# Optimization experiments

Measured on AMD Instinct MI355X. Metric: run time of the kernel, lower is better.

Reference implementation:

```python
import jax, jax.numpy as jnp
import numpy as np

NUM_USERS = 1024
NUM_BUSINESSES = 2048
N_NODES = NUM_USERS + NUM_BUSINESSES  # 3072
B = 1024            # batch size (== NUM_USERS to keep the business_idx-offset bug valid)
E = 16384           # edges (self loops added inside reference, PyG GATConv default)
H = 768             # hidden_size
HEADS = 8
NUM_IMAGES = 3


def setup_inputs() -> dict:
    key = jax.random.key(0)
    ks = jax.random.split(key, 24)
    def rn(k, shape, s=0.02):
        return jax.random.normal(k, shape, dtype=jnp.float32) * s
    inp = {
        'text_cls': rn(ks[0], (B, 768), 1.0),              # BERT CLS features
        'img_cls': rn(ks[1], (B, NUM_IMAGES, 768), 1.0),   # ViT CLS features per image
        'biz_feats': rn(ks[2], (B, 3), 1.0),
        'W_text': rn(ks[3], (768, H)), 'b_text': jnp.zeros((H,), jnp.float32),
        'W_img': rn(ks[4], (768, H)), 'b_img': jnp.zeros((H,), jnp.float32),
        'W_bf': rn(ks[5], (3, H)), 'b_bf': jnp.zeros((H,), jnp.float32),
        'user_table': rn(ks[6], (NUM_USERS, H)),
        'biz_table': rn(ks[7], (NUM_BUSINESSES, H)),
        'W1': rn(ks[8], (H, HEADS * H)),
        'att_src1': rn(ks[9], (HEADS, H), 0.1),
        'att_dst1': rn(ks[10], (HEADS, H), 0.1),
        'b1': jnp.zeros((HEADS * H,), jnp.float32),
        'W2': rn(ks[11], (HEADS * H, H)),
        'att_src2': rn(ks[12], (1, H), 0.1),
        'att_dst2': rn(ks[13], (1, H), 0.1),
        'b2': jnp.zeros((H,), jnp.float32),
        'Wf1': rn(ks[14], (4 * H, 2 * H)), 'bf1': jnp.zeros((2 * H,), jnp.float32),
        'Wf2': rn(ks[15], (2 * H, H)), 'bf2': jnp.zeros((H,), jnp.float32),
        'Wf3': rn(ks[16], (H, 1)), 'bf3': jnp.zeros((1,), jnp.float32),
        'user_idx': jax.random.randint(ks[17], (B,), 0, NUM_USERS),
        'business_idx': jax.random.randint(ks[18], (B,), NUM_USERS, N_NODES),
        'edge_index': jax.random.randint(ks[19], (2, E), 0, N_NODES),
    }
    return inp


def gat_conv(x, src, dst, W, a_src, a_dst, bias, heads):
    # PyG GATConv: linear -> per-head additive attention -> scatter softmax over dst -> scatter add
    N = x.shape[0]
    C = W.shape[1] // heads
    h = (x @ W).reshape(N, heads, C)                       # [N,H,C]
    s_src = jnp.sum(h * a_src, axis=-1)                    # [N,H]
    s_dst = jnp.sum(h * a_dst, axis=-1)                    # [N,H]
    e = jax.nn.leaky_relu(s_src[src] + s_dst[dst], 0.2)    # [E,H]
    e_max = jax.ops.segment_max(e, dst, num_segments=N)    # [N,H]
    ee = jnp.exp(e - e_max[dst])
    denom = jax.ops.segment_sum(ee, dst, num_segments=N)   # [N,H]
    alpha = ee / (denom[dst] + 1e-16)                      # [E,H]
    out = jax.ops.segment_sum(h[src] * alpha[..., None], dst, num_segments=N)  # [N,H,C]
    return out.reshape(N, heads * C) + bias


def reference(text_cls, img_cls, biz_feats, W_text, b_text, W_img, b_img, W_bf, b_bf,
              user_table, biz_table, W1, att_src1, att_dst1, b1, W2, att_src2, att_dst2, b2,
              Wf1, bf1, Wf2, bf2, Wf3, bf3, user_idx, business_idx, edge_index):
    text_emb = text_cls @ W_text + b_text                       # TextEncoder.fc
    img_emb = jnp.mean(img_cls, axis=1) @ W_img + b_img         # ImageEncoder mean + fc
    meta = biz_feats @ W_bf + b_bf                              # business_feature_fc
    user_emb = user_table[user_idx]
    biz_emb = biz_table[business_idx - user_idx.shape[0]]       # faithful: offset by batch size
    x = jnp.zeros((N_NODES, H), jnp.float32)
    x = x.at[user_idx].set(user_emb)
    x = x.at[business_idx].set((text_emb + img_emb + meta + biz_emb) / 4.0)
    loop = jnp.arange(N_NODES)
    src = jnp.concatenate([edge_index[0], loop])                # add self loops (PyG default)
    dst = jnp.concatenate([edge_index[1], loop])
    x = jax.nn.relu(gat_conv(x, src, dst, W1, att_src1, att_dst1, b1, HEADS))
    x = gat_conv(x, src, dst, W2, att_src2, att_dst2, b2, 1)
    cat = jnp.concatenate([x[user_idx], x[business_idx], text_emb, img_emb], axis=1)  # [B,4H]
    h1 = jax.nn.relu(cat @ Wf1 + bf1)
    h2 = jax.nn.relu(h1 @ Wf2 + bf2)
    return (h2 @ Wf3 + bf3).squeeze(-1)                         # [B]
```

## Files before the change

### kernel.cpp

```cpp
#include <hip/hip_runtime.h>
#include <hip/hip_bf16.h>

namespace {

constexpr int kB = 1024;
constexpr int kNU = 1024;
constexpr int kNB = 2048;
constexpr int kNN = 3072;
constexpr int kE = 16384;
constexpr int kET = kE + kNN;
constexpr int kH = 768;
constexpr int kHeads = 8;
constexpr int kSplitK = 4;

typedef __attribute__((ext_vector_type(8))) short bf16x8_t;
typedef __attribute__((ext_vector_type(4))) float f32x4_t;

__device__ __forceinline__ float tof(float x) { return x; }
__device__ __forceinline__ float tof(__hip_bfloat16 x) { return __bfloat162float(x); }
__device__ __forceinline__ void stor(float* p, float v) { *p = v; }
__device__ __forceinline__ void stor(__hip_bfloat16* p, float v) { *p = __float2bfloat16(v); }

__device__ __forceinline__ float blo(unsigned u) {
  union { unsigned u; float f; } c; c.u = u << 16; return c.f;
}
__device__ __forceinline__ float bhi(unsigned u) {
  union { unsigned u; float f; } c; c.u = u & 0xffff0000u; return c.f;
}

__device__ __forceinline__ unsigned pk2(float a, float b) {
  union { __hip_bfloat16 h[2]; unsigned u; } c;
  c.h[0] = __float2bfloat16(a); c.h[1] = __float2bfloat16(b);
  return c.u;
}

__device__ __forceinline__ void gload_lds16(const void* g, void* l) {
  __builtin_amdgcn_global_load_lds(
      (const __attribute__((address_space(1))) void*)g,
      (__attribute__((address_space(3))) void*)l, 16, 0, 0);
}

template <int BM, int BN, int FM, int FN, typename TC>
__device__ __forceinline__ void gemm_body(
    const __hip_bfloat16* __restrict__ A, const __hip_bfloat16* __restrict__ Bt,
    const float* __restrict__ bias, TC* __restrict__ C,
    int K, int lda, int ldc, int act, int bx, int by) {
  __shared__ __align__(16) __hip_bfloat16 As[2][BM][32];
  __shared__ __align__(16) __hip_bfloat16 Bs[2][BN][32];
  const int t = threadIdx.x;
  const int w = t >> 6, lane = t & 63;
  const int wm = w >> 1, wn = w & 1;
  const int bm = by * BM, bn = bx * BN;
  const int lr = lane & 15, lg = lane >> 4;

  f32x4_t acc[FM][FN];
#pragma unroll
  for (int m = 0; m < FM; ++m)
#pragma unroll
    for (int n = 0; n < FN; ++n) acc[m][n] = (f32x4_t){0.f, 0.f, 0.f, 0.f};

  auto stage = [&](int buf, int kt) {
    const int k0 = kt << 5;
#pragma unroll
    for (int i = 0; i < BM / 64; ++i) {
      int L = i * 256 + t;
      gload_lds16(A + (size_t)(bm + (L >> 2)) * lda + k0 + (L & 3) * 8,
                  (char*)(&As[buf][0][0]) + ((size_t)(i * 256 + w * 64)) * 16);
    }
#pragma unroll
    for (int i = 0; i < BN / 64; ++i) {
      int L = i * 256 + t;
      gload_lds16(Bt + (size_t)(bn + (L >> 2)) * K + k0 + (L & 3) * 8,
                  (char*)(&Bs[buf][0][0]) + ((size_t)(i * 256 + w * 64)) * 16);
    }
  };

  const int NT = K >> 5;
  stage(0, 0);
  __syncthreads();
  for (int kt = 0; kt < NT; ++kt) {
    const int cur = kt & 1;
    if (kt + 1 < NT) stage(cur ^ 1, kt + 1);
    bf16x8_t af[FM], bv[FN];
#pragma unroll
    for (int m = 0; m < FM; ++m)
      af[m] = *(const bf16x8_t*)&As[cur][wm * FM * 16 + m * 16 + lr][lg * 8];
#pragma unroll
    for (int n = 0; n < FN; ++n)
      bv[n] = *(const bf16x8_t*)&Bs[cur][wn * FN * 16 + n * 16 + lr][lg * 8];
#pragma unroll
    for (int m = 0; m < FM; ++m)
#pragma unroll
      for (int n = 0; n < FN; ++n)
        acc[m][n] = __builtin_amdgcn_mfma_f32_16x16x32_bf16(af[m], bv[n], acc[m][n], 0, 0, 0);
    __syncthreads();
  }

#pragma unroll
  for (int m = 0; m < FM; ++m) {
    const int row0 = bm + wm * FM * 16 + m * 16 + lg * 4;
#pragma unroll
    for (int n = 0; n < FN; ++n) {
      const int cn = bn + wn * FN * 16 + n * 16 + lr;
      const float bvv = bias ? bias[cn] : 0.f;
#pragma unroll
      for (int r = 0; r < 4; ++r) {
        float v = acc[m][n][r] + bvv;
        if (act) v = fmaxf(v, 0.f);
        stor(&C[(size_t)(row0 + r) * ldc + cn], v);
      }
    }
  }
}

__device__ __forceinline__ void swz_xy(bool mfast, int& bx, int& by) {
  const int nwg = gridDim.x * gridDim.y;
  const int orig = blockIdx.y * gridDim.x + blockIdx.x;
  const int swz = (orig & 7) * (nwg >> 3) + (orig >> 3);
  if (mfast) { by = swz % gridDim.y; bx = swz / gridDim.y; }
  else       { bx = swz % gridDim.x; by = swz / gridDim.x; }
}

template <int BM, int BN, int FM, int FN, typename TC, bool MFAST>
__global__ __launch_bounds__(256) void mfma_gemm(
    const __hip_bfloat16* __restrict__ A, const __hip_bfloat16* __restrict__ Bt,
    const float* __restrict__ bias, TC* __restrict__ C,
    int N, int K, int act) {
  int bx, by;
  swz_xy(MFAST, bx, by);
  gemm_body<BM, BN, FM, FN, TC>(A, Bt, bias, C, K, K, N, act, bx, by);
}

template <int BM, int BN, int FM, int FN>
__global__ __launch_bounds__(256) void mfma_gemm_dual(
    const __hip_bfloat16* __restrict__ A0, const __hip_bfloat16* __restrict__ Bt0,
    const float* __restrict__ bias0, float* __restrict__ C0,
    const __hip_bfloat16* __restrict__ A1, const __hip_bfloat16* __restrict__ Bt1,
    const float* __restrict__ bias1, float* __restrict__ C1,
    int N, int K) {
  int bx, by;
  swz_xy(true, bx, by);
  const __hip_bfloat16* A = blockIdx.z ? A1 : A0;
  const __hip_bfloat16* Bt = blockIdx.z ? Bt1 : Bt0;
  const float* bias = blockIdx.z ? bias1 : bias0;
  float* C = blockIdx.z ? C1 : C0;
  gemm_body<BM, BN, FM, FN, float>(A, Bt, bias, C, K, K, N, 0, bx, by);
}

template <int BM, int BN, int FM, int FN>
__global__ __launch_bounds__(256) void gemm_head(
    const __hip_bfloat16* __restrict__ y, const __hip_bfloat16* __restrict__ W1t,
    const float* __restrict__ b1, __hip_bfloat16* __restrict__ x2) {
  int bx, by;
  swz_xy(true, bx, by);
  const int hd = blockIdx.z;
  gemm_body<BM, BN, FM, FN, __hip_bfloat16>(
      y + (size_t)hd * kH, W1t + (size_t)hd * kH * kH, b1 + hd * kH,
      x2 + (size_t)hd * kH, kH, kHeads * kH, kHeads * kH, 1, bx, by);
}

template <int BM, int BN, int FM, int FN>
__global__ __launch_bounds__(256) void mfma_gemm_splitk(
    const __hip_bfloat16* __restrict__ A, const __hip_bfloat16* __restrict__ Bt,
    float* __restrict__ Cpart, int M, int N, int K, int KC) {
  __shared__ __align__(16) __hip_bfloat16 As[2][BM][32];
  __shared__ __align__(16) __hip_bfloat16 Bs[2][BN][32];
  int bx, by;
  swz_xy(false, bx, by);
  const int t = threadIdx.x;
  const int w = t >> 6, lane = t & 63;
  const int wm = w >> 1, wn = w & 1;
  const int bm = by * BM, bn = bx * BN;
  const int kbeg = blockIdx.z * KC;
  const int lr = lane & 15, lg = lane >> 4;

  f32x4_t acc[FM][FN];
#pragma unroll
  for (int m = 0; m < FM; ++m)
#pragma unroll
    for (int n = 0; n < FN; ++n) acc[m][n] = (f32x4_t){0.f, 0.f, 0.f, 0.f};

  auto stage = [&](int buf, int kt) {
    const int k0 = kbeg + (kt << 5);
#pragma unroll
    for (int i = 0; i < BM / 64; ++i) {
      int L = i * 256 + t;
      gload_lds16(A + (size_t)(bm + (L >> 2)) * K + k0 + (L & 3) * 8,
                  (char*)(&As[buf][0][0]) + ((size_t)(i * 256 + w * 64)) * 16);
    }
#pragma unroll
    for (int i = 0; i < BN / 64; ++i) {
      int L = i * 256 + t;
      gload_lds16(Bt + (size_t)(bn + (L >> 2)) * K + k0 + (L & 3) * 8,
                  (char*)(&Bs[buf][0][0]) + ((size_t)(i * 256 + w * 64)) * 16);
    }
  };

  const int NT = KC >> 5;
  stage(0, 0);
  __syncthreads();
  for (int kt = 0; kt < NT; ++kt) {
    const int cur = kt & 1;
    if (kt + 1 < NT) stage(cur ^ 1, kt + 1);
    bf16x8_t af[FM], bv[FN];
#pragma unroll
    for (int m = 0; m < FM; ++m)
      af[m] = *(const bf16x8_t*)&As[cur][wm * FM * 16 + m * 16 + lr][lg * 8];
#pragma unroll
    for (int n = 0; n < FN; ++n)
      bv[n] = *(const bf16x8_t*)&Bs[cur][wn * FN * 16 + n * 16 + lr][lg * 8];
#pragma unroll
    for (int m = 0; m < FM; ++m)
#pragma unroll
      for (int n = 0; n < FN; ++n)
        acc[m][n] = __builtin_amdgcn_mfma_f32_16x16x32_bf16(af[m], bv[n], acc[m][n], 0, 0, 0);
    __syncthreads();
  }

  float* Cp = Cpart + (size_t)blockIdx.z * M * N;
#pragma unroll
  for (int m = 0; m < FM; ++m) {
    const int row0 = bm + wm * FM * 16 + m * 16 + lg * 4;
#pragma unroll
    for (int n = 0; n < FN; ++n) {
      const int cn = bn + wn * FN * 16 + n * 16 + lr;
#pragma unroll
      for (int r = 0; r < 4; ++r) Cp[(size_t)(row0 + r) * N + cn] = acc[m][n][r];
    }
  }
}

__global__ __launch_bounds__(192) void reduce_scores2_kernel(
    const float* __restrict__ part, const float* __restrict__ att_src,
    const float* __restrict__ att_dst, __hip_bfloat16* __restrict__ h2,
    float* __restrict__ s_src, float* __restrict__ s_dst) {
  __shared__ float redS[3], redD[3];
  const int row = blockIdx.x;
  const int t = threadIdx.x;
  const int c = t * 4;
  const float* p = part + (size_t)row * kH + c;
  float4 s = *(const float4*)p;
#pragma unroll
  for (int z = 1; z < kSplitK; ++z) {
    float4 qv = *(const float4*)(p + (size_t)z * kNN * kH);
    s.x += qv.x; s.y += qv.y; s.z += qv.z; s.w += qv.w;
  }
  __hip_bfloat16 b0 = __float2bfloat16(s.x), b1 = __float2bfloat16(s.y);
  __hip_bfloat16 b2 = __float2bfloat16(s.z), b3 = __float2bfloat16(s.w);
  __hip_bfloat16* o = h2 + (size_t)row * kH + c;
  o[0] = b0; o[1] = b1; o[2] = b2; o[3] = b3;
  float f0 = tof(b0), f1 = tof(b1), f2 = tof(b2), f3 = tof(b3);
  float ss = f0 * att_src[c] + f1 * att_src[c + 1] + f2 * att_src[c + 2] + f3 * att_src[c + 3];
  float sd = f0 * att_dst[c] + f1 * att_dst[c + 1] + f2 * att_dst[c + 2] + f3 * att_dst[c + 3];
#pragma unroll
  for (int off = 32; off; off >>= 1) { ss += __shfl_down(ss, off); sd += __shfl_down(sd, off); }
  if ((t & 63) == 0) { redS[t >> 6] = ss; redD[t >> 6] = sd; }
  __syncthreads();
  if (t == 0) {
    s_src[row] = redS[0] + redS[1] + redS[2];
    s_dst[row] = redD[0] + redD[1] + redD[2];
  }
}

struct TJobs {
  const float* in[6];
  __hip_bfloat16* out[6];
  int K[6];
  int N[6];
  int start[7];
};

__global__ __launch_bounds__(256) void transp_prep_kernel(
    TJobs j, const float* __restrict__ text_cls, const float* __restrict__ img_cls,
    __hip_bfloat16* __restrict__ text_bf, __hip_bfloat16* __restrict__ imgm_bf) {
  __shared__ float tl[32][33];
  const int bid = blockIdx.x;
  const int t = threadIdx.x;
  if (bid >= j.start[6]) {
    int idx = (bid - j.start[6]) * 256 + t;
    if (idx < kB * kH) {
      text_bf[idx] = __float2bfloat16(text_cls[idx]);
      int b = idx / kH, c = idx - b * kH;
      const float* p = img_cls + (size_t)b * 3 * kH + c;
      imgm_bf[idx] = __float2bfloat16((p[0] + p[kH] + p[2 * kH]) * (1.f / 3.f));
    }
    return;
  }
  int idx = 0;
#pragma unroll
  for (int q = 1; q < 6; ++q)
    if (bid >= j.start[q]) idx = q;
  const int tile = bid - j.start[idx];
  const int N = j.N[idx], K = j.K[idx];
  const int tilesN = N >> 5;
  const int n0 = (tile % tilesN) << 5, k0 = (tile / tilesN) << 5;
  const float* in = j.in[idx];
  __hip_bfloat16* out = j.out[idx];
  const int r = t >> 3, c = (t & 7) * 4;
#pragma unroll
  for (int i = 0; i < 4; ++i) tl[r][c + i] = in[(size_t)(k0 + r) * N + n0 + c + i];
  __syncthreads();
  __hip_bfloat16* op = out + (size_t)(n0 + r) * K + k0 + c;
#pragma unroll
  for (int i = 0; i < 4; ++i) op[i] = __float2bfloat16(tl[c + i][r]);
}

__global__ __launch_bounds__(256) void wa1_kernel(const float* __restrict__ W1,
                                                  const float* __restrict__ a_src,
                                                  const float* __restrict__ a_dst,
                                                  float* __restrict__ wa) {
  int gw = (blockIdx.x * 256 + threadIdx.x) >> 6;
  int lane = threadIdx.x & 63;
  if (gw >= kHeads * kH) return;
  int i = gw >> 3, hd = gw & 7;
  const float* wrow = W1 + (size_t)i * (kHeads * kH) + hd * kH;
  const float* as = a_src + (size_t)hd * kH;
  const float* ad = a_dst + (size_t)hd * kH;
  float ss = 0.f, sd = 0.f;
  for (int c = lane; c < kH; c += 64) {
    float wv = wrow[c];
    ss = fmaf(wv, as[c], ss);
    sd = fmaf(wv, ad[c], sd);
  }
#pragma unroll
  for (int o = 32; o; o >>= 1) { ss += __shfl_down(ss, o); sd += __shfl_down(sd, o); }
  if (lane == 0) {
    wa[hd * kH + i] = ss;
    wa[kHeads * kH + hd * kH + i] = sd;
  }
}

__global__ __launch_bounds__(256) void s1_kernel(const __hip_bfloat16* __restrict__ xb,
                                                 const float* __restrict__ wa,
                                                 float* __restrict__ s1s,
                                                 float* __restrict__ s1d) {
  __shared__ unsigned xrow[kH / 2];
  const int n = blockIdx.x;
  const int t = threadIdx.x;
  const unsigned* xp = (const unsigned*)(xb + (size_t)n * kH);
  if (t < 128) { xrow[t] = xp[t]; xrow[t + 128] = xp[t + 128]; xrow[t + 256] = xp[t + 256]; }
  __syncthreads();
  const int w = t >> 6, lane = t & 63;
  const float* ws0 = wa + (size_t)w * kH;
  const float* wd0 = wa + (size_t)(kHeads + w) * kH;
  const float* ws1 = wa + (size_t)(w + 4) * kH;
  const float* wd1 = wa + (size_t)(kHeads + w + 4) * kH;
  float s0 = 0.f, d0 = 0.f, s1 = 0.f, d1 = 0.f;
  for (int u = lane; u < kH / 2; u += 64) {
    unsigned v = xrow[u];
    float f0 = blo(v), f1 = bhi(v);
    int c = u * 2;
    s0 = fmaf(f0, ws0[c], fmaf(f1, ws0[c + 1], s0));
    d0 = fmaf(f0, wd0[c], fmaf(f1, wd0[c + 1], d0));
    s1 = fmaf(f0, ws1[c], fmaf(f1, ws1[c + 1], s1));
    d1 = fmaf(f0, wd1[c], fmaf(f1, wd1[c + 1], d1));
  }
#pragma unroll
  for (int o = 32; o; o >>= 1) {
    s0 += __shfl_down(s0, o); d0 += __shfl_down(d0, o);
    s1 += __shfl_down(s1, o); d1 += __shfl_down(d1, o);
  }
  if (lane == 0) {
    s1s[n * 8 + w] = s0;     s1d[n * 8 + w] = d0;
    s1s[n * 8 + w + 4] = s1; s1d[n * 8 + w + 4] = d1;
  }
}

__global__ __launch_bounds__(256) void agg1x_kernel(
    const int* __restrict__ rowptr, const int* __restrict__ cols,
    const float* __restrict__ s1s, const float* __restrict__ s1d,
    const __hip_bfloat16* __restrict__ xb, __hip_bfloat16* __restrict__ y) {
  __shared__ float mh[8], rdh[8], sdl[8];
  __shared__ float alph[128][9];
  const int n = blockIdx.x;
  const int t = threadIdx.x, w = t >> 6, lane = t & 63;
  const int beg = rowptr[n], end = rowptr[n + 1];
  if (t < 8) sdl[t] = s1d[n * 8 + t];
  __syncthreads();
#pragma unroll
  for (int p = 0; p < 2; ++p) {
    const int h = w + p * 4;
    const float sd = sdl[h];
    float m = -3.402823466e38f;
    for (int i = beg + lane; i < end; i += 64) {
      float e = s1s[(size_t)cols[i] * 8 + h] + sd;
      e = (e > 0.f) ? e : 0.2f * e;
      m = fmaxf(m, e);
    }
#pragma unroll
    for (int o = 32; o; o >>= 1) m = fmaxf(m, __shfl_xor(m, o));
    float ds = 0.f;
    for (int i = beg + lane; i < end; i += 64) {
      float e = s1s[(size_t)cols[i] * 8 + h] + sd;
      e = (e > 0.f) ? e : 0.2f * e;
      ds += expf(e - m);
    }
#pragma unroll
    for (int o = 32; o; o >>= 1) ds += __shfl_xor(ds, o);
    if (lane == 0) { mh[h] = m; rdh[h] = 1.f / (ds + 1e-16f); }
  }
  __syncthreads();

  float acc[8][4];
#pragma unroll
  for (int h = 0; h < 8; ++h)
#pragma unroll
    for (int q = 0; q < 4; ++q) acc[h][q] = 0.f;
  const int c0 = t * 4;

  for (int chunk = beg; chunk < end; chunk += 128) {
    const int cnt = min(128, end - chunk);
#pragma unroll
    for (int p = 0; p < 2; ++p) {
      const int h = w + p * 4;
      const float sd = sdl[h], m = mh[h], rd = rdh[h];
      for (int i = lane; i < cnt; i += 64) {
        float e = s1s[(size_t)cols[chunk + i] * 8 + h] + sd;
        e = (e > 0.f) ? e : 0.2f * e;
        alph[i][h] = expf(e - m) * rd;
      }
    }
    __syncthreads();
    if (t < 192) {
      for (int i = 0; i < cnt; ++i) {
        int src = cols[chunk + i];
        uint2 v = *(const uint2*)(xb + (size_t)src * kH + c0);
        float f0 = blo(v.x), f1 = bhi(v.x), f2 = blo(v.y), f3 = bhi(v.y);
#pragma unroll
        for (int h = 0; h < 8; ++h) {
          float a = alph[i][h];
          acc[h][0] = fmaf(a, f0, acc[h][0]);
          acc[h][1] = fmaf(a, f1, acc[h][1]);
          acc[h][2] = fmaf(a, f2, acc[h][2]);
          acc[h][3] = fmaf(a, f3, acc[h][3]);
        }
      }
    }
    __syncthreads();
  }
  if (t < 192) {
#pragma unroll
    for (int h = 0; h < 8; ++h) {
      uint2 o;
      o.x = pk2(acc[h][0], acc[h][1]);
      o.y = pk2(acc[h][2], acc[h][3]);
      *(uint2*)(y + ((size_t)n * 8 + h) * kH + c0) = o;
    }
  }
}

__global__ void init_kernel(uint4* __restrict__ xb4, int* __restrict__ deg,
                            int* __restrict__ winner) {
  int i = blockIdx.x * 256 + threadIdx.x;
  if (i < kNN * kH * 2 / 16) xb4[i] = (uint4){0u, 0u, 0u, 0u};
  if (i < kNN) deg[i] = 0;
  if (i < kNB) winner[i] = -1;
}

__global__ void deg_winner_kernel(const int* __restrict__ ei, int* __restrict__ deg,
                                  const int* __restrict__ business_idx,
                                  int* __restrict__ winner) {
  int e = blockIdx.x * 256 + threadIdx.x;
  if (e < kET) {
    int dst = (e < kE) ? ei[kE + e] : (e - kE);
    atomicAdd(&deg[dst], 1);
  }
  if (e < kB) atomicMax(&winner[business_idx[e] - kNU], e);
}

__global__ __launch_bounds__(1024) void scan_kernel(const int* __restrict__ deg,
                                                    int* __restrict__ rowptr,
                                                    int* __restrict__ cursor) {
  __shared__ int sums[1024];
  int t = threadIdx.x;
  int v0 = deg[t * 3], v1 = deg[t * 3 + 1], v2 = deg[t * 3 + 2];
  int s = v0 + v1 + v2;
  sums[t] = s;
  __syncthreads();
  for (int o = 1; o < 1024; o <<= 1) {
    int xv = (t >= o) ? sums[t - o] : 0;
    __syncthreads();
    sums[t] += xv;
    __syncthreads();
  }
  int excl = sums[t] - s;
  rowptr[t * 3] = excl;          cursor[t * 3] = excl;
  rowptr[t * 3 + 1] = excl + v0; cursor[t * 3 + 1] = excl + v0;
  rowptr[t * 3 + 2] = excl + v0 + v1; cursor[t * 3 + 2] = excl + v0 + v1;
  if (t == 1023) rowptr[kNN] = excl + s;
}

__global__ void fill_kernel(const int* __restrict__ ei, int* __restrict__ cursor,
                            int* __restrict__ cols) {
  int e = blockIdx.x * 256 + threadIdx.x;
  if (e >= kET) return;
  int src, dst;
  if (e < kE) { src = ei[e]; dst = ei[kE + e]; } else { src = dst = e - kE; }
  int pos = atomicAdd(&cursor[dst], 1);
  cols[pos] = src;
}

__global__ void build_x_kernel(const int* __restrict__ user_idx,
                               const float* __restrict__ user_table,
                               const int* __restrict__ winner,
                               const float* __restrict__ text_emb,
                               const float* __restrict__ img_emb,
                               const float* __restrict__ biz_feats,
                               const float* __restrict__ W_bf,
                               const float* __restrict__ b_bf,
                               const float* __restrict__ biz_table,
                               __hip_bfloat16* __restrict__ xb) {
  int b = blockIdx.x;
  if (b < kNU) {
    int node = user_idx[b];
    for (int c = threadIdx.x; c < kH; c += blockDim.x)
      xb[(size_t)node * kH + c] = __float2bfloat16(user_table[(size_t)node * kH + c]);
  } else {
    int m = b - kNU;
    int w = winner[m];
    if (w < 0) return;
    int node = kNU + m;
    float f0 = biz_feats[w * 3], f1 = biz_feats[w * 3 + 1], f2 = biz_feats[w * 3 + 2];
    for (int c = threadIdx.x; c < kH; c += blockDim.x) {
      float meta = f0 * W_bf[c] + f1 * W_bf[kH + c] + f2 * W_bf[2 * kH + c] + b_bf[c];
      float v = (text_emb[(size_t)w * kH + c] + img_emb[(size_t)w * kH + c] + meta +
                 biz_table[(size_t)m * kH + c]) * 0.25f;
      xb[(size_t)node * kH + c] = __float2bfloat16(v);
    }
  }
}

__global__ __launch_bounds__(256) void gat_agg_kernel(
    const int* __restrict__ rowptr, const int* __restrict__ cols,
    const float* __restrict__ s_src, const float* __restrict__ s_dst,
    const __hip_bfloat16* __restrict__ h, const float* __restrict__ bias,
    float* __restrict__ out_f, int total) {
  const int pair = blockIdx.x * 4 + (threadIdx.x >> 6);
  if (pair >= total) return;
  const int lane = threadIdx.x & 63;
  const int n = pair;
  const int beg = rowptr[n], end = rowptr[n + 1];
  const float sdv = s_dst[pair];

  float m = -3.402823466e38f;
  for (int i = beg + lane; i < end; i += 64) {
    float e = s_src[cols[i]] + sdv;
    e = (e > 0.f) ? e : 0.2f * e;
    m = fmaxf(m, e);
  }
#pragma unroll
  for (int o = 32; o; o >>= 1) m = fmaxf(m, __shfl_xor(m, o));

  float dsum = 0.f;
  for (int i = beg + lane; i < end; i += 64) {
    float e = s_src[cols[i]] + sdv;
    e = (e > 0.f) ? e : 0.2f * e;
    dsum += expf(e - m);
  }
#pragma unroll
  for (int o = 32; o; o >>= 1) dsum += __shfl_xor(dsum, o);
  const float rdsum = 1.f / (dsum + 1e-16f);

  float a[12];
#pragma unroll
  for (int q = 0; q < 12; ++q) a[q] = 0.f;
  const size_t hoff = (size_t)lane * 4;
  for (int i = beg; i < end; ++i) {
    int src = cols[i];
    float e = s_src[src] + sdv;
    e = (e > 0.f) ? e : 0.2f * e;
    float wgt = expf(e - m) * rdsum;
    const __hip_bfloat16* hp = h + (size_t)src * kH + hoff;
#pragma unroll
    for (int j = 0; j < 3; ++j) {
      uint2 v = *(const uint2*)(hp + j * 256);
      a[j * 4 + 0] = fmaf(wgt, blo(v.x), a[j * 4 + 0]);
      a[j * 4 + 1] = fmaf(wgt, bhi(v.x), a[j * 4 + 1]);
      a[j * 4 + 2] = fmaf(wgt, blo(v.y), a[j * 4 + 2]);
      a[j * 4 + 3] = fmaf(wgt, bhi(v.y), a[j * 4 + 3]);
    }
  }
  const size_t ob = (size_t)n * kH + hoff;
#pragma unroll
  for (int j = 0; j < 3; ++j) {
#pragma unroll
    for (int q = 0; q < 4; ++q)
      out_f[ob + j * 256 + q] = a[j * 4 + q] + bias[hoff + j * 256 + q];
  }
}

__global__ void cat_kernel(const float* __restrict__ xf, const float* __restrict__ text_emb,
                           const float* __restrict__ img_emb, const int* __restrict__ user_idx,
                           const int* __restrict__ business_idx, __hip_bfloat16* __restrict__ cat) {
  int b = blockIdx.x;
  int u = user_idx[b], z = business_idx[b];
  __hip_bfloat16* crow = cat + (size_t)b * 4 * kH;
  for (int c = threadIdx.x; c < kH; c += blockDim.x) {
    crow[c] = __float2bfloat16(xf[(size_t)u * kH + c]);
    crow[kH + c] = __float2bfloat16(xf[(size_t)z * kH + c]);
    crow[2 * kH + c] = __float2bfloat16(text_emb[(size_t)b * kH + c]);
    crow[3 * kH + c] = __float2bfloat16(img_emb[(size_t)b * kH + c]);
  }
}

__global__ __launch_bounds__(256) void final_kernel(const float* __restrict__ m2,
                                                    const float* __restrict__ Wf3,
                                                    const float* __restrict__ bf3,
                                                    float* __restrict__ out) {
  int b = (blockIdx.x * 256 + threadIdx.x) >> 6;
  int lane = threadIdx.x & 63;
  if (b >= kB) return;
  float s = 0.f;
  for (int c = lane; c < kH; c += 64) s = fmaf(m2[(size_t)b * kH + c], Wf3[c], s);
#pragma unroll
  for (int o = 32; o; o >>= 1) s += __shfl_down(s, o);
  if (lane == 0) out[b] = s + bf3[0];
}

}

extern "C" void kernel_launch(void* const* d_in, const int* in_sizes, int n_in,
                              void* d_out, int out_size, void* d_ws, size_t ws_size,
                              hipStream_t stream) {
  const float* text_cls = (const float*)d_in[0];
  const float* img_cls = (const float*)d_in[1];
  const float* biz_feats = (const float*)d_in[2];
  const float* W_text = (const float*)d_in[3];
  const float* b_text = (const float*)d_in[4];
  const float* W_img = (const float*)d_in[5];
  const float* b_img = (const float*)d_in[6];
  const float* W_bf = (const float*)d_in[7];
  const float* b_bf = (const float*)d_in[8];
  const float* user_table = (const float*)d_in[9];
  const float* biz_table = (const float*)d_in[10];
  const float* W1 = (const float*)d_in[11];
  const float* att_src1 = (const float*)d_in[12];
  const float* att_dst1 = (const float*)d_in[13];
  const float* b1 = (const float*)d_in[14];
  const float* W2 = (const float*)d_in[15];
  const float* att_src2 = (const float*)d_in[16];
  const float* att_dst2 = (const float*)d_in[17];
  const float* b2 = (const float*)d_in[18];
  const float* Wf1 = (const float*)d_in[19];
  const float* bf1 = (const float*)d_in[20];
  const float* Wf2 = (const float*)d_in[21];
  const float* bf2 = (const float*)d_in[22];
  const float* Wf3 = (const float*)d_in[23];
  const float* bf3 = (const float*)d_in[24];
  const int* user_idx = (const int*)d_in[25];
  const int* business_idx = (const int*)d_in[26];
  const int* edge_index = (const int*)d_in[27];
  float* out = (float*)d_out;
  (void)in_sizes; (void)n_in; (void)out_size; (void)ws_size;

  char* base = (char*)d_ws;
  size_t off = 0;
  auto alloc = [&](size_t bytes) -> void* {
    void* p = base + off;
    off = (off + bytes + 255) & ~(size_t)255;
    return p;
  };
  __hip_bfloat16* xb = (__hip_bfloat16*)alloc((size_t)kNN * kH * 2);
  __hip_bfloat16* text_bf = (__hip_bfloat16*)alloc((size_t)kB * kH * 2);
  __hip_bfloat16* imgm_bf = (__hip_bfloat16*)alloc((size_t)kB * kH * 2);
  float* text_emb = (float*)alloc((size_t)kB * kH * 4);
  float* img_emb = (float*)alloc((size_t)kB * kH * 4);
  __hip_bfloat16* Wtt = (__hip_bfloat16*)alloc((size_t)kH * kH * 2);
  __hip_bfloat16* Wit = (__hip_bfloat16*)alloc((size_t)kH * kH * 2);
  __hip_bfloat16* W1t = (__hip_bfloat16*)alloc((size_t)kHeads * kH * kH * 2);
  __hip_bfloat16* W2t = (__hip_bfloat16*)alloc((size_t)kH * kHeads * kH * 2);
  __hip_bfloat16* Wf1t = (__hip_bfloat16*)alloc((size_t)2 * kH * 4 * kH * 2);
  __hip_bfloat16* Wf2t = (__hip_bfloat16*)alloc((size_t)kH * 2 * kH * 2);
  float* wa = (float*)alloc((size_t)2 * kHeads * kH * 4);
  __hip_bfloat16* y = (__hip_bfloat16*)alloc((size_t)kNN * kHeads * kH * 2);
  __hip_bfloat16* x2 = (__hip_bfloat16*)alloc((size_t)kNN * kHeads * kH * 2);
  __hip_bfloat16* h2 = (__hip_bfloat16*)alloc((size_t)kNN * kH * 2);
  float* xf = (float*)alloc((size_t)kNN * kH * 4);
  float* s1s = (float*)alloc((size_t)kNN * kHeads * 4);
  float* s1d = (float*)alloc((size_t)kNN * kHeads * 4);
  float* s2s = (float*)alloc((size_t)kNN * 4);
  float* s2d = (float*)alloc((size_t)kNN * 4);
  __hip_bfloat16* catb = (__hip_bfloat16*)alloc((size_t)kB * 4 * kH * 2);
  __hip_bfloat16* m1 = (__hip_bfloat16*)alloc((size_t)kB * 2 * kH * 2);
  float* m2 = (float*)alloc((size_t)kB * kH * 4);
  int* deg = (int*)alloc((size_t)kNN * 4);
  int* rowptr = (int*)alloc((size_t)(kNN + 1) * 4);
  int* cursor = (int*)alloc((size_t)kNN * 4);
  int* cols = (int*)alloc((size_t)kET * 4);
  int* winner = (int*)alloc((size_t)kNB * 4);

  float* part = (float*)y;

  init_kernel<<<(kNN * kH * 2 / 16 + 255) / 256, 256, 0, stream>>>((uint4*)xb, deg, winner);

  TJobs tj;
  tj.in[0] = W_text; tj.out[0] = Wtt;  tj.K[0] = kH;          tj.N[0] = kH;
  tj.in[1] = W_img;  tj.out[1] = Wit;  tj.K[1] = kH;          tj.N[1] = kH;
  tj.in[2] = W1;     tj.out[2] = W1t;  tj.K[2] = kH;          tj.N[2] = kHeads * kH;
  tj.in[3] = W2;     tj.out[3] = W2t;  tj.K[3] = kHeads * kH; tj.N[3] = kH;
  tj.in[4] = Wf1;    tj.out[4] = Wf1t; tj.K[4] = 4 * kH;      tj.N[4] = 2 * kH;
  tj.in[5] = Wf2;    tj.out[5] = Wf2t; tj.K[5] = 2 * kH;      tj.N[5] = kH;
  tj.start[0] = 0;
  for (int q = 0; q < 6; ++q)
    tj.start[q + 1] = tj.start[q] + (tj.K[q] / 32) * (tj.N[q] / 32);
  const int prep_blocks = (kB * kH + 255) / 256;
  transp_prep_kernel<<<tj.start[6] + prep_blocks, 256, 0, stream>>>(tj, text_cls, img_cls,
                                                                    text_bf, imgm_bf);

  wa1_kernel<<<(kHeads * kH) / 4, 256, 0, stream>>>(W1, att_src1, att_dst1, wa);

  mfma_gemm_dual<64, 128, 2, 4><<<dim3(kH / 128, kB / 64, 2), 256, 0, stream>>>(
      text_bf, Wtt, b_text, text_emb, imgm_bf, Wit, b_img, img_emb, kH, kH);

  deg_winner_kernel<<<(kET + 255) / 256, 256, 0, stream>>>(edge_index, deg, business_idx, winner);
  scan_kernel<<<1, 1024, 0, stream>>>(deg, rowptr, cursor);
  fill_kernel<<<(kET + 255) / 256, 256, 0, stream>>>(edge_index, cursor, cols);

  build_x_kernel<<<kNN, 256, 0, stream>>>(user_idx, user_table, winner, text_emb, img_emb,
                                          biz_feats, W_bf, b_bf, biz_table, xb);

  s1_kernel<<<kNN, 256, 0, stream>>>(xb, wa, s1s, s1d);
  agg1x_kernel<<<kNN, 256, 0, stream>>>(rowptr, cols, s1s, s1d, xb, y);
  gemm_head<128, 128, 4, 4><<<dim3(kH / 128, kNN / 128, kHeads), 256, 0, stream>>>(
      y, W1t, b1, x2);

  mfma_gemm_splitk<64, 128, 2, 4><<<dim3(kH / 128, kNN / 64, kSplitK), 256, 0, stream>>>(
      x2, W2t, part, kNN, kH, kHeads * kH, kHeads * kH / kSplitK);
  reduce_scores2_kernel<<<kNN, 192, 0, stream>>>(part, att_src2, att_dst2, h2, s2s, s2d);
  gat_agg_kernel<<<kNN / 4, 256, 0, stream>>>(rowptr, cols, s2s, s2d, h2, b2, xf, kNN);

  cat_kernel<<<kB, 256, 0, stream>>>(xf, text_emb, img_emb, user_idx, business_idx, catb);
  mfma_gemm<64, 128, 2, 4, __hip_bfloat16, true><<<dim3(2 * kH / 128, kB / 64), 256, 0, stream>>>(
      catb, Wf1t, bf1, m1, 2 * kH, 4 * kH, 1);
  mfma_gemm<64, 64, 2, 2, float, true><<<dim3(kH / 64, kB / 64), 256, 0, stream>>>(
      m1, Wf2t, bf2, m2, kH, 2 * kH, 1);
  final_kernel<<<(kB * 64 + 255) / 256, 256, 0, stream>>>(m2, Wf3, bf3, out);
}
```

Measured before the change: 305.7 us.

## Split-K the MLP head GEMMs, fuse final dot, merge wa1 into prep kernel

Replaces the two MLP-head GEMMs with split-K (2-way) GEMMs writing fp32 partials, adds a reduce+bias+relu kernel after the first and a reduce+bias+relu+Wf3-dot kernel that replaces the separate final kernel. The wa1 attention-weight precompute is folded into the transpose/prep launch as extra blocks, and gemm_head's grid is reordered so heads are the fastest-varying block index. The aim is more blocks for the small 1024-row GEMMs, fewer launches, and different L2 locality for the head GEMM. The cost is extra fp32 partial traffic and reduction passes.

```diff
diff --git a/kernel.cpp b/kernel.cpp
--- a/kernel.cpp
+++ b/kernel.cpp
@@ -151,9 +151,10 @@
 __global__ __launch_bounds__(256) void gemm_head(
     const __hip_bfloat16* __restrict__ y, const __hip_bfloat16* __restrict__ W1t,
     const float* __restrict__ b1, __hip_bfloat16* __restrict__ x2) {
-  int bx, by;
-  swz_xy(true, bx, by);
-  const int hd = blockIdx.z;
+  const int hd = blockIdx.x;
+  const int tile = blockIdx.y;
+  const int bx = tile % (kH / BN);
+  const int by = tile / (kH / BN);
   gemm_body<BM, BN, FM, FN, __hip_bfloat16>(
       y + (size_t)hd * kH, W1t + (size_t)hd * kH * kH, b1 + hd * kH,
       x2 + (size_t)hd * kH, kH, kHeads * kH, kHeads * kH, 1, bx, by);
@@ -262,6 +263,47 @@
   }
 }
 
+__global__ void reduce_relu_kernel(const float* __restrict__ part,
+                                   const float* __restrict__ bias,
+                                   __hip_bfloat16* __restrict__ outb, int MN4, int N) {
+  int i = blockIdx.x * 256 + threadIdx.x;
+  if (i >= MN4) return;
+  float4 s = ((const float4*)part)[i];
+  float4 p = ((const float4*)part)[(size_t)MN4 + i];
+  int c = (i * 4) % N;
+  float v0 = fmaxf(s.x + p.x + bias[c], 0.f);
+  float v1 = fmaxf(s.y + p.y + bias[c + 1], 0.f);
+  float v2 = fmaxf(s.z + p.z + bias[c + 2], 0.f);
+  float v3 = fmaxf(s.w + p.w + bias[c + 3], 0.f);
+  uint2 o;
+  o.x = pk2(v0, v1); o.y = pk2(v2, v3);
+  *(uint2*)(outb + (size_t)i * 4) = o;
+}
+
+__global__ __launch_bounds__(192) void reduce_final_kernel(
+    const float* __restrict__ part, const float* __restrict__ bias,
+    const float* __restrict__ Wf3, const float* __restrict__ bf3,
+    float* __restrict__ out) {
+  __shared__ float red[3];
+  const int row = blockIdx.x;
+  const int t = threadIdx.x;
+  const int c = t * 4;
+  const float* p0 = part + (size_t)row * kH + c;
+  const float* p1 = p0 + (size_t)kB * kH;
+  float4 a = *(const float4*)p0;
+  float4 b = *(const float4*)p1;
+  float v0 = fmaxf(a.x + b.x + bias[c], 0.f);
+  float v1 = fmaxf(a.y + b.y + bias[c + 1], 0.f);
+  float v2 = fmaxf(a.z + b.z + bias[c + 2], 0.f);
+  float v3 = fmaxf(a.w + b.w + bias[c + 3], 0.f);
+  float s = v0 * Wf3[c] + v1 * Wf3[c + 1] + v2 * Wf3[c + 2] + v3 * Wf3[c + 3];
+#pragma unroll
+  for (int off = 32; off; off >>= 1) s += __shfl_down(s, off);
+  if ((t & 63) == 0) red[t >> 6] = s;
+  __syncthreads();
+  if (t == 0) out[row] = red[0] + red[1] + red[2] + bf3[0];
+}
+
 struct TJobs {
   const float* in[6];
   __hip_bfloat16* out[6];
@@ -272,10 +314,34 @@
 
 __global__ __launch_bounds__(256) void transp_prep_kernel(
     TJobs j, const float* __restrict__ text_cls, const float* __restrict__ img_cls,
-    __hip_bfloat16* __restrict__ text_bf, __hip_bfloat16* __restrict__ imgm_bf) {
+    __hip_bfloat16* __restrict__ text_bf, __hip_bfloat16* __restrict__ imgm_bf,
+    int prep_blocks, const float* __restrict__ W1, const float* __restrict__ a_src,
+    const float* __restrict__ a_dst, float* __restrict__ wa) {
   __shared__ float tl[32][33];
   const int bid = blockIdx.x;
   const int t = threadIdx.x;
+  if (bid >= j.start[6] + prep_blocks) {
+    int gw = ((bid - j.start[6] - prep_blocks) * 256 + t) >> 6;
+    int lane = t & 63;
+    if (gw >= kHeads * kH) return;
+    int i = gw >> 3, hd = gw & 7;
+    const float* wrow = W1 + (size_t)i * (kHeads * kH) + hd * kH;
+    const float* as = a_src + (size_t)hd * kH;
+    const float* ad = a_dst + (size_t)hd * kH;
+    float ss = 0.f, sd = 0.f;
+    for (int c = lane; c < kH; c += 64) {
+      float wv = wrow[c];
+      ss = fmaf(wv, as[c], ss);
+      sd = fmaf(wv, ad[c], sd);
+    }
+#pragma unroll
+    for (int o = 32; o; o >>= 1) { ss += __shfl_down(ss, o); sd += __shfl_down(sd, o); }
+    if (lane == 0) {
+      wa[hd * kH + i] = ss;
+      wa[kHeads * kH + hd * kH + i] = sd;
+    }
+    return;
+  }
   if (bid >= j.start[6]) {
     int idx = (bid - j.start[6]) * 256 + t;
     if (idx < kB * kH) {
@@ -303,31 +369,6 @@
   __hip_bfloat16* op = out + (size_t)(n0 + r) * K + k0 + c;
 #pragma unroll
   for (int i = 0; i < 4; ++i) op[i] = __float2bfloat16(tl[c + i][r]);
-}
-
-__global__ __launch_bounds__(256) void wa1_kernel(const float* __restrict__ W1,
-                                                  const float* __restrict__ a_src,
-                                                  const float* __restrict__ a_dst,
-                                                  float* __restrict__ wa) {
-  int gw = (blockIdx.x * 256 + threadIdx.x) >> 6;
-  int lane = threadIdx.x & 63;
-  if (gw >= kHeads * kH) return;
-  int i = gw >> 3, hd = gw & 7;
-  const float* wrow = W1 + (size_t)i * (kHeads * kH) + hd * kH;
-  const float* as = a_src + (size_t)hd * kH;
-  const float* ad = a_dst + (size_t)hd * kH;
-  float ss = 0.f, sd = 0.f;
-  for (int c = lane; c < kH; c += 64) {
-    float wv = wrow[c];
-    ss = fmaf(wv, as[c], ss);
-    sd = fmaf(wv, ad[c], sd);
-  }
-#pragma unroll
-  for (int o = 32; o; o >>= 1) { ss += __shfl_down(ss, o); sd += __shfl_down(sd, o); }
-  if (lane == 0) {
-    wa[hd * kH + i] = ss;
-    wa[kHeads * kH + hd * kH + i] = sd;
-  }
 }
 
 __global__ __launch_bounds__(256) void s1_kernel(const __hip_bfloat16* __restrict__ xb,
@@ -601,20 +642,6 @@
     crow[2 * kH + c] = __float2bfloat16(text_emb[(size_t)b * kH + c]);
     crow[3 * kH + c] = __float2bfloat16(img_emb[(size_t)b * kH + c]);
   }
-}
-
-__global__ __launch_bounds__(256) void final_kernel(const float* __restrict__ m2,
-                                                    const float* __restrict__ Wf3,
-                                                    const float* __restrict__ bf3,
-                                                    float* __restrict__ out) {
-  int b = (blockIdx.x * 256 + threadIdx.x) >> 6;
-  int lane = threadIdx.x & 63;
-  if (b >= kB) return;
-  float s = 0.f;
-  for (int c = lane; c < kH; c += 64) s = fmaf(m2[(size_t)b * kH + c], Wf3[c], s);
-#pragma unroll
-  for (int o = 32; o; o >>= 1) s += __shfl_down(s, o);
-  if (lane == 0) out[b] = s + bf3[0];
 }
 
 }
@@ -688,6 +715,7 @@
   int* cursor = (int*)alloc((size_t)kNN * 4);
   int* cols = (int*)alloc((size_t)kET * 4);
   int* winner = (int*)alloc((size_t)kNB * 4);
+  (void)m2;
 
   float* part = (float*)y;
 
@@ -704,10 +732,9 @@
   for (int q = 0; q < 6; ++q)
     tj.start[q + 1] = tj.start[q] + (tj.K[q] / 32) * (tj.N[q] / 32);
   const int prep_blocks = (kB * kH + 255) / 256;
-  transp_prep_kernel<<<tj.start[6] + prep_blocks, 256, 0, stream>>>(tj, text_cls, img_cls,
-                                                                    text_bf, imgm_bf);
-
-  wa1_kernel<<<(kHeads * kH) / 4, 256, 0, stream>>>(W1, att_src1, att_dst1, wa);
+  const int wa_blocks = (kHeads * kH) / 4;
+  transp_prep_kernel<<<tj.start[6] + prep_blocks + wa_blocks, 256, 0, stream>>>(
+      tj, text_cls, img_cls, text_bf, imgm_bf, prep_blocks, W1, att_src1, att_dst1, wa);
 
   mfma_gemm_dual<64, 128, 2, 4><<<dim3(kH / 128, kB / 64, 2), 256, 0, stream>>>(
       text_bf, Wtt, b_text, text_emb, imgm_bf, Wit, b_img, img_emb, kH, kH);
@@ -721,7 +748,7 @@
 
   s1_kernel<<<kNN, 256, 0, stream>>>(xb, wa, s1s, s1d);
   agg1x_kernel<<<kNN, 256, 0, stream>>>(rowptr, cols, s1s, s1d, xb, y);
-  gemm_head<128, 128, 4, 4><<<dim3(kH / 128, kNN / 128, kHeads), 256, 0, stream>>>(
+  gemm_head<128, 128, 4, 4><<<dim3(kHeads, (kNN / 128) * (kH / 128)), 256, 0, stream>>>(
       y, W1t, b1, x2);
 
   mfma_gemm_splitk<64, 128, 2, 4><<<dim3(kH / 128, kNN / 64, kSplitK), 256, 0, stream>>>(
@@ -730,9 +757,11 @@
   gat_agg_kernel<<<kNN / 4, 256, 0, stream>>>(rowptr, cols, s2s, s2d, h2, b2, xf, kNN);
 
   cat_kernel<<<kB, 256, 0, stream>>>(xf, text_emb, img_emb, user_idx, business_idx, catb);
-  mfma_gemm<64, 128, 2, 4, __hip_bfloat16, true><<<dim3(2 * kH / 128, kB / 64), 256, 0, stream>>>(
-      catb, Wf1t, bf1, m1, 2 * kH, 4 * kH, 1);
-  mfma_gemm<64, 64, 2, 2, float, true><<<dim3(kH / 64, kB / 64), 256, 0, stream>>>(
-      m1, Wf2t, bf2, m2, kH, 2 * kH, 1);
-  final_kernel<<<(kB * 64 + 255) / 256, 256, 0, stream>>>(m2, Wf3, bf3, out);
-}
+  mfma_gemm_splitk<64, 128, 2, 4><<<dim3(2 * kH / 128, kB / 64, 2), 256, 0, stream>>>(
+      catb, Wf1t, part, kB, 2 * kH, 4 * kH, 2 * kH);
+  reduce_relu_kernel<<<(kB * 2 * kH / 4 + 255) / 256, 256, 0, stream>>>(
+      part, bf1, m1, kB * 2 * kH / 4, 2 * kH);
+  mfma_gemm_splitk<64, 128, 2, 4><<<dim3(kH / 128, kB / 64, 2), 256, 0, stream>>>(
+      m1, Wf2t, part, kB, kH, 2 * kH, kH);
+  reduce_final_kernel<<<kB, 192, 0, stream>>>(part, bf2, Wf3, bf3, out);
+}
```

After: 270.7 us. 11.4% less time.
